# Optimization experiments

Hardware: AMD Instinct MI355X
Metric: run time of the kernel (lower is better)

## Reference

```python
import jax, jax.numpy as jnp
import numpy as np

B, C, H, W = 8, 128, 256, 256
KERNELS = [1, 3, 5]


def _dwconv(x, w, k):
    # depthwise conv, groups == channels, padding k//2 (SAME for odd k)
    return jax.lax.conv_general_dilated(
        x, w, window_strides=(1, 1),
        padding=[(k // 2, k // 2), (k // 2, k // 2)],
        dimension_numbers=("NCHW", "OIHW", "NCHW"),
        feature_group_count=x.shape[1])


def setup_inputs() -> dict:
    key = jax.random.key(0)
    ks = jax.random.split(key, 5)
    x = jax.random.normal(ks[0], (B, C, H, W), jnp.float32)
    # depthwise weights: torch layout [out_ch, in_ch/groups, k, k] = [4C, 1, k, k]
    w1 = jax.random.normal(ks[1], (4 * C, 1, 1, 1), jnp.float32) * 0.2
    w3 = jax.random.normal(ks[2], (4 * C, 1, 3, 3), jnp.float32) * 0.1
    w5 = jax.random.normal(ks[3], (4 * C, 1, 5, 5), jnp.float32) * 0.05
    # proj 1x1 conv: [4C, 12C, 1, 1]
    w_proj = jax.random.normal(ks[4], (4 * C, 12 * C, 1, 1), jnp.float32) * 0.02
    return {"x": x, "w1": w1, "w3": w3, "w5": w5, "w_proj": w_proj}


def reference(x, w1, w3, w5, w_proj):
    # DWT: strided split -> channel concat  [B,C,H,W] -> [B,4C,H/2,W/2]
    xd = jnp.concatenate([
        x[:, :, 0::2, 0::2], x[:, :, 0::2, 1::2],
        x[:, :, 1::2, 0::2], x[:, :, 1::2, 1::2]], axis=1)
    # multi-kernel depthwise convs, concat -> [B,12C,H/2,W/2]
    feats = jnp.concatenate([
        _dwconv(xd, w1, 1), _dwconv(xd, w3, 3), _dwconv(xd, w5, 5)], axis=1)
    # 1x1 projection: [B,12C,h,w] -> [B,4C,h,w]
    y = jnp.einsum("bchw,oc->bohw", feats, w_proj[:, :, 0, 0])
    # IDWT: strided zero-scatter back to [B,C,H,W]
    c = y.shape[1] // 4
    ll, lh, hl, hh = jnp.split(y, 4, axis=1)
    out = jnp.zeros((y.shape[0], c, y.shape[2] * 2, y.shape[3] * 2), y.dtype)
    out = (out.at[:, :, 0::2, 0::2].set(ll)
              .at[:, :, 0::2, 1::2].set(lh)
              .at[:, :, 1::2, 0::2].set(hl)
              .at[:, :, 1::2, 1::2].set(hh))
    return out
```

## Files before the change

### kernel.cpp

```cpp
#include <hip/hip_runtime.h>
#include <hip/hip_bf16.h>
#include <stdint.h>

typedef __bf16 bf16_t;
typedef __bf16 bf16x8 __attribute__((ext_vector_type(8)));
typedef float f32x4 __attribute__((ext_vector_type(4)));

constexpr int CC = 128, HH = 256, WW = 256;
constexpr int C4 = 512, K12 = 1536;
constexpr int AWP_ELEMS = 786432;
constexpr int LW2_ELEMS = 512 * 40;

__global__ __launch_bounds__(256)
void prep(const float* __restrict__ wp, const float* __restrict__ w1,
          const float* __restrict__ w3, const float* __restrict__ w5,
          bf16_t* __restrict__ awp, float* __restrict__ lw2g)
{
    int t = blockIdx.x * 256 + threadIdx.x;
    if (t < AWP_ELEMS) {
        int kk = t & 31, o = (t >> 5) & 511, t2 = t >> 14;
        int g = t2 >> 4, cb = t2 & 15;
        awp[t] = (bf16_t)wp[o * K12 + g * C4 + cb * 32 + kk];
        return;
    }
    int u = t - AWP_ELEMS;
    if (u < LW2_ELEMS) {
        int c4 = u / 40, j = u - c4 * 40;
        int r = j >> 3, v = j & 7;
        float val = 0.f;
        if (v < 5)                 val = w5[c4 * 25 + r * 5 + v];
        else if (r >= 1 && r <= 3) val = w3[c4 * 9 + (r - 1) * 3 + (v - 5)];
        else if (r == 0 && v == 5) val = w1[c4];
        lw2g[u] = val;
    }
}

__device__ __forceinline__ void gload4(const float* g, float* l) {
    __builtin_amdgcn_global_load_lds(
        (const __attribute__((address_space(1))) uint32_t*)g,
        (__attribute__((address_space(3))) uint32_t*)l, 4, 0, 0);
}

__device__ __forceinline__ int bt_off(int row, int colbyte) {
    int f = ((row >> 1) ^ (row >> 2)) & 7;
    return row * 256 + (colbyte ^ (f << 4));
}

__device__ __forceinline__ uint16_t b16bits(float v) {
    return __builtin_bit_cast(uint16_t, (bf16_t)v);
}

__global__ __launch_bounds__(1024, 4)
void wtconv_mfma(const float* __restrict__ x,
                 const bf16_t* __restrict__ awp,
                 const float* __restrict__ lw2g,
                 float* __restrict__ out)
{
    __shared__ __align__(16) float lx[32][5][136];
    __shared__ __align__(16) char  BtB[128 * 256];
    __shared__ __align__(16) float lw2s[2][1280];

    const int tid = threadIdx.x;
    const int lane = tid & 63;
    const int wid = __builtin_amdgcn_readfirstlane(tid >> 6);
    const int nb = blockIdx.x;
    const int m = (nb & 7) * 128 + (nb >> 3);
    const int b = m >> 7, i = m & 127;
    const int wm = wid & 7, wn = wid >> 3;
    const int lrow = lane & 15, lkh = lane >> 4;
    const float* xb = x + (size_t)b * CC * HH * WW;

    for (int e = tid; e < 32 * 5 * 136 / 4; e += 1024)
        ((f32x4*)lx)[e] = (f32x4){0.f, 0.f, 0.f, 0.f};
    __syncthreads();

    f32x4 acc[4][4];
#pragma unroll
    for (int a = 0; a < 4; ++a)
#pragma unroll
        for (int c = 0; c < 4; ++c) acc[a][c] = (f32x4){0.f, 0.f, 0.f, 0.f};

    auto issue_lx = [&](int cb) {
        const int q4 = cb >> 2;
        const int qy = q4 >> 1, qx = q4 & 1;
        const int bcb = (cb & 3) * 32;
#pragma unroll
        for (int cl = 0; cl < 2; ++cl) {
            const int chan = wid * 2 + cl;
#pragma unroll
            for (int r = 0; r < 5; ++r) {
                const int ri = i + r - 2;
                if ((unsigned)ri < 128u) {
#pragma unroll
                    for (int h = 0; h < 2; ++h) {
                        const float* s = xb + (((size_t)(bcb + chan)) << 16)
                                       + (2 * ri + qy) * WW + qx + h * 128;
                        gload4(s + 2 * lane, &lx[chan][r][2 + h * 64]);
                    }
                }
            }
        }
    };
    auto issue_lw = [&](int cb, int buf) {
        const float* src = lw2g + cb * 1280;
        float* dst = lw2s[buf];
#pragma unroll 1
        for (int t = wid; t < 20; t += 16)
            gload4(src + t * 64 + lane, dst + t * 64);
    };

    issue_lw(0, 0);
    issue_lx(0);

    const int pxq = tid & 31;
    const int chan = (tid >> 5) & 31;
    const int px0 = pxq * 4;

#pragma unroll 1
    for (int cb = 0; cb < 16; ++cb) {
        __syncthreads();

        const int buf = cb & 1;
        const float* wrow = &lw2s[buf][chan * 40];
        float f5[4] = {0.f,0.f,0.f,0.f}, f3[4] = {0.f,0.f,0.f,0.f}, f1[4];
        float w1v = 0.f;
#pragma unroll
        for (int r = 0; r < 5; ++r) {
            f32x4 wA = *(const f32x4*)(wrow + r * 8);
            f32x4 wB = *(const f32x4*)(wrow + r * 8 + 4);
            f32x4 a  = *(const f32x4*)&lx[chan][r][px0];
            f32x4 bv = *(const f32x4*)&lx[chan][r][px0 + 4];
            float col[8] = {a[0],a[1],a[2],a[3],bv[0],bv[1],bv[2],bv[3]};
            if (r == 0) w1v = wB[1];
#pragma unroll
            for (int d = 0; d < 4; ++d)
                f5[d] += wA[0]*col[d] + wA[1]*col[d+1] + wA[2]*col[d+2]
                       + wA[3]*col[d+3] + wB[0]*col[d+4];
            if (r >= 1 && r <= 3) {
#pragma unroll
                for (int d = 0; d < 4; ++d)
                    f3[d] += wB[1]*col[d+1] + wB[2]*col[d+2] + wB[3]*col[d+3];
            }
            if (r == 2) {
#pragma unroll
                for (int d = 0; d < 4; ++d) f1[d] = w1v * col[d + 2];
            }
        }
#pragma unroll
        for (int d = 0; d < 4; ++d) {
            const int row = px0 + d;
            const int cby = chan * 2;
            *(uint16_t*)&BtB[bt_off(row, cby)]       = b16bits(f1[d]);
            *(uint16_t*)&BtB[bt_off(row, 64 + cby)]  = b16bits(f3[d]);
            *(uint16_t*)&BtB[bt_off(row, 128 + cby)] = b16bits(f5[d]);
        }
        __syncthreads();

        if (cb < 15) { issue_lw(cb + 1, (cb + 1) & 1); issue_lx(cb + 1); }

#pragma unroll 1
        for (int g = 0; g < 3; ++g) {
            bf16x8 bfrag[4];
#pragma unroll
            for (int nf = 0; nf < 4; ++nf) {
                const int row = wn * 64 + nf * 16 + lrow;
                bfrag[nf] = *(const bf16x8*)&BtB[bt_off(row, g * 64 + lkh * 16)];
            }
            const bf16_t* abase = awp + (size_t)(g * 16 + cb) * (512 * 32);
#pragma unroll
            for (int mf = 0; mf < 4; ++mf) {
                const int o = wm * 64 + mf * 16 + lrow;
                bf16x8 af = *(const bf16x8*)(abase + o * 32 + lkh * 8);
#pragma unroll
                for (int nf = 0; nf < 4; ++nf)
                    acc[mf][nf] = __builtin_amdgcn_mfma_f32_16x16x32_bf16(
                        af, bfrag[nf], acc[mf][nf], 0, 0, 0);
            }
        }
    }

    const int oy = 2 * i + (wm >> 2);
    const int ox = (wm >> 1) & 1;
#pragma unroll
    for (int mf = 0; mf < 4; ++mf)
#pragma unroll
        for (int nf = 0; nf < 4; ++nf)
#pragma unroll
            for (int r = 0; r < 4; ++r) {
                const int bco = (wm & 1) * 64 + mf * 16 + lkh * 4 + r;
                const int px  = wn * 64 + nf * 16 + lrow;
                out[((size_t)(b * CC + bco) * HH + oy) * WW + 2 * px + ox]
                    = acc[mf][nf][r];
            }
}

extern "C" void kernel_launch(void* const* d_in, const int* in_sizes, int n_in,
                              void* d_out, int out_size, void* d_ws, size_t ws_size,
                              hipStream_t stream) {
    const float* x  = (const float*)d_in[0];
    const float* w1 = (const float*)d_in[1];
    const float* w3 = (const float*)d_in[2];
    const float* w5 = (const float*)d_in[3];
    const float* wp = (const float*)d_in[4];
    float* out = (float*)d_out;
    bf16_t* awp = (bf16_t*)d_ws;
    float* lw2g = (float*)((char*)d_ws + (size_t)AWP_ELEMS * 2);

    int prep_total = AWP_ELEMS + LW2_ELEMS;
    hipLaunchKernelGGL(prep, dim3((prep_total + 255) / 256), dim3(256), 0, stream,
                       wp, w1, w3, w5, awp, lw2g);
    hipLaunchKernelGGL(wtconv_mfma, dim3(1024), dim3(1024), 0, stream,
                       x, awp, lw2g, out);
}
```

Measured before the change: 536.8 us.

## Warp-specialize depthwise producer and double-buffer Bt tile to overlap with MFMA

Splits the block's waves so only the first 8 waves compute the depthwise convolutions, 8 output pixels per thread, and load the next stage's inputs. All waves run MFMA on the previous stage's tile from a double-buffered Bt LDS area, with one barrier per iteration instead of two. The projection weight layout is interleaved so the three kernel sizes of a channel sit next to each other in K, and the bf16 writes to LDS are packed into 32-bit stores. The aim is to overlap the depthwise VALU work with matrix ops and cut synchronization. In exchange it uses more LDS, which may lower occupancy, and half the waves sit idle during the depthwise phase.

```diff
diff --git a/kernel.cpp b/kernel.cpp
--- a/kernel.cpp
+++ b/kernel.cpp
@@ -9,7 +9,7 @@
 constexpr int CC = 128, HH = 256, WW = 256;
 constexpr int C4 = 512, K12 = 1536;
 constexpr int AWP_ELEMS = 786432;
-constexpr int LW2_ELEMS = 512 * 40;
+constexpr int LW2_ELEMS = 512 * 48;
 
 __global__ __launch_bounds__(256)
 void prep(const float* __restrict__ wp, const float* __restrict__ w1,
@@ -18,19 +18,23 @@
 {
     int t = blockIdx.x * 256 + threadIdx.x;
     if (t < AWP_ELEMS) {
-        int kk = t & 31, o = (t >> 5) & 511, t2 = t >> 14;
-        int g = t2 >> 4, cb = t2 & 15;
-        awp[t] = (bf16_t)wp[o * K12 + g * C4 + cb * 32 + kk];
+        int kl = t % 96;
+        int o  = (t / 96) & 511;
+        int cb = t / (96 * 512);
+        int chan = kl / 3, g = kl - chan * 3;
+        awp[t] = (bf16_t)wp[o * K12 + g * C4 + cb * 32 + chan];
         return;
     }
     int u = t - AWP_ELEMS;
     if (u < LW2_ELEMS) {
-        int c4 = u / 40, j = u - c4 * 40;
+        int c4 = u / 48, j = u - c4 * 48;
         int r = j >> 3, v = j & 7;
         float val = 0.f;
-        if (v < 5)                 val = w5[c4 * 25 + r * 5 + v];
-        else if (r >= 1 && r <= 3) val = w3[c4 * 9 + (r - 1) * 3 + (v - 5)];
-        else if (r == 0 && v == 5) val = w1[c4];
+        if (j < 40) {
+            if (v < 5)                 val = w5[c4 * 25 + r * 5 + v];
+            else if (r >= 1 && r <= 3) val = w3[c4 * 9 + (r - 1) * 3 + (v - 5)];
+            else if (r == 0 && v == 5) val = w1[c4];
+        }
         lw2g[u] = val;
     }
 }
@@ -40,14 +44,11 @@
         (const __attribute__((address_space(1))) uint32_t*)g,
         (__attribute__((address_space(3))) uint32_t*)l, 4, 0, 0);
 }
-
-__device__ __forceinline__ int bt_off(int row, int colbyte) {
-    int f = ((row >> 1) ^ (row >> 2)) & 7;
-    return row * 256 + (colbyte ^ (f << 4));
-}
-
 __device__ __forceinline__ uint16_t b16bits(float v) {
     return __builtin_bit_cast(uint16_t, (bf16_t)v);
+}
+__device__ __forceinline__ uint32_t pk2(float a, float b) {
+    return (uint32_t)b16bits(a) | ((uint32_t)b16bits(b) << 16);
 }
 
 __global__ __launch_bounds__(1024, 4)
@@ -56,9 +57,9 @@
                  const float* __restrict__ lw2g,
                  float* __restrict__ out)
 {
-    __shared__ __align__(16) float lx[32][5][136];
-    __shared__ __align__(16) char  BtB[128 * 256];
-    __shared__ __align__(16) float lw2s[2][1280];
+    __shared__ __align__(16) float lx[32][5][140];
+    __shared__ __align__(16) char  BtB[2][128 * 256];
+    __shared__ __align__(16) float lw2s[32][48];
 
     const int tid = threadIdx.x;
     const int lane = tid & 63;
@@ -70,7 +71,7 @@
     const int lrow = lane & 15, lkh = lane >> 4;
     const float* xb = x + (size_t)b * CC * HH * WW;
 
-    for (int e = tid; e < 32 * 5 * 136 / 4; e += 1024)
+    for (int e = tid; e < 32 * 5 * 140 / 4; e += 1024)
         ((f32x4*)lx)[e] = (f32x4){0.f, 0.f, 0.f, 0.f};
     __syncthreads();
 
@@ -80,101 +81,109 @@
 #pragma unroll
         for (int c = 0; c < 4; ++c) acc[a][c] = (f32x4){0.f, 0.f, 0.f, 0.f};
 
-    auto issue_lx = [&](int cb) {
-        const int q4 = cb >> 2;
-        const int qy = q4 >> 1, qx = q4 & 1;
-        const int bcb = (cb & 3) * 32;
-#pragma unroll
-        for (int cl = 0; cl < 2; ++cl) {
-            const int chan = wid * 2 + cl;
+    auto issue_own = [&](int kk) {
+        const int q4 = kk >> 2, qy = q4 >> 1, qx = q4 & 1;
+        const int bcb = (kk & 3) * 32;
+#pragma unroll
+        for (int cl = 0; cl < 4; ++cl) {
+            const int chan = wid * 4 + cl;
 #pragma unroll
             for (int r = 0; r < 5; ++r) {
                 const int ri = i + r - 2;
                 if ((unsigned)ri < 128u) {
-#pragma unroll
-                    for (int h = 0; h < 2; ++h) {
-                        const float* s = xb + (((size_t)(bcb + chan)) << 16)
-                                       + (2 * ri + qy) * WW + qx + h * 128;
-                        gload4(s + 2 * lane, &lx[chan][r][2 + h * 64]);
-                    }
-                }
-            }
-        }
+                    const float* s = xb + (((size_t)(bcb + chan)) << 16)
+                                   + (2 * ri + qy) * WW + qx;
+                    gload4(s + 2 * lane,       &lx[chan][r][2]);
+                    gload4(s + 128 + 2 * lane, &lx[chan][r][66]);
+                }
+            }
+        }
+        const float* wsrc = lw2g + kk * 1536 + wid * 192;
+        float* wdst = &lw2s[wid * 4][0];
+#pragma unroll
+        for (int t = 0; t < 3; ++t)
+            gload4(wsrc + t * 64 + lane, wdst + t * 64);
     };
-    auto issue_lw = [&](int cb, int buf) {
-        const float* src = lw2g + cb * 1280;
-        float* dst = lw2s[buf];
+
+    if (wid < 8) issue_own(0);
+
+    const int chan = (tid >> 4) & 31;
+    const int oct = tid & 15;
+    const int px0 = oct * 8;
+
 #pragma unroll 1
-        for (int t = wid; t < 20; t += 16)
-            gload4(src + t * 64 + lane, dst + t * 64);
-    };
-
-    issue_lw(0, 0);
-    issue_lx(0);
-
-    const int pxq = tid & 31;
-    const int chan = (tid >> 5) & 31;
-    const int px0 = pxq * 4;
-
-#pragma unroll 1
-    for (int cb = 0; cb < 16; ++cb) {
+    for (int k = 0; k <= 16; ++k) {
         __syncthreads();
 
-        const int buf = cb & 1;
-        const float* wrow = &lw2s[buf][chan * 40];
-        float f5[4] = {0.f,0.f,0.f,0.f}, f3[4] = {0.f,0.f,0.f,0.f}, f1[4];
-        float w1v = 0.f;
-#pragma unroll
-        for (int r = 0; r < 5; ++r) {
-            f32x4 wA = *(const f32x4*)(wrow + r * 8);
-            f32x4 wB = *(const f32x4*)(wrow + r * 8 + 4);
-            f32x4 a  = *(const f32x4*)&lx[chan][r][px0];
-            f32x4 bv = *(const f32x4*)&lx[chan][r][px0 + 4];
-            float col[8] = {a[0],a[1],a[2],a[3],bv[0],bv[1],bv[2],bv[3]};
-            if (r == 0) w1v = wB[1];
-#pragma unroll
-            for (int d = 0; d < 4; ++d)
-                f5[d] += wA[0]*col[d] + wA[1]*col[d+1] + wA[2]*col[d+2]
-                       + wA[3]*col[d+3] + wB[0]*col[d+4];
-            if (r >= 1 && r <= 3) {
-#pragma unroll
-                for (int d = 0; d < 4; ++d)
-                    f3[d] += wB[1]*col[d+1] + wB[2]*col[d+2] + wB[3]*col[d+3];
-            }
-            if (r == 2) {
-#pragma unroll
-                for (int d = 0; d < 4; ++d) f1[d] = w1v * col[d + 2];
-            }
-        }
-#pragma unroll
-        for (int d = 0; d < 4; ++d) {
-            const int row = px0 + d;
-            const int cby = chan * 2;
-            *(uint16_t*)&BtB[bt_off(row, cby)]       = b16bits(f1[d]);
-            *(uint16_t*)&BtB[bt_off(row, 64 + cby)]  = b16bits(f3[d]);
-            *(uint16_t*)&BtB[bt_off(row, 128 + cby)] = b16bits(f5[d]);
-        }
-        __syncthreads();
-
-        if (cb < 15) { issue_lw(cb + 1, (cb + 1) & 1); issue_lx(cb + 1); }
-
-#pragma unroll 1
-        for (int g = 0; g < 3; ++g) {
-            bf16x8 bfrag[4];
-#pragma unroll
-            for (int nf = 0; nf < 4; ++nf) {
-                const int row = wn * 64 + nf * 16 + lrow;
-                bfrag[nf] = *(const bf16x8*)&BtB[bt_off(row, g * 64 + lkh * 16)];
-            }
-            const bf16_t* abase = awp + (size_t)(g * 16 + cb) * (512 * 32);
-#pragma unroll
-            for (int mf = 0; mf < 4; ++mf) {
-                const int o = wm * 64 + mf * 16 + lrow;
-                bf16x8 af = *(const bf16x8*)(abase + o * 32 + lkh * 8);
-#pragma unroll
-                for (int nf = 0; nf < 4; ++nf)
-                    acc[mf][nf] = __builtin_amdgcn_mfma_f32_16x16x32_bf16(
-                        af, bfrag[nf], acc[mf][nf], 0, 0, 0);
+        if (wid < 8 && k < 16) {
+            const float* wr = &lw2s[chan][0];
+            float f5[8] = {0,0,0,0,0,0,0,0}, f3[8] = {0,0,0,0,0,0,0,0}, f1[8];
+            float w1v = 0.f;
+#pragma unroll
+            for (int r = 0; r < 5; ++r) {
+                f32x4 wA = *(const f32x4*)(wr + r * 8);
+                f32x4 wB = *(const f32x4*)(wr + r * 8 + 4);
+                f32x4 v0 = *(const f32x4*)&lx[chan][r][px0];
+                f32x4 v1 = *(const f32x4*)&lx[chan][r][px0 + 4];
+                f32x4 v2 = *(const f32x4*)&lx[chan][r][px0 + 8];
+                float c[12] = {v0[0],v0[1],v0[2],v0[3], v1[0],v1[1],v1[2],v1[3],
+                               v2[0],v2[1],v2[2],v2[3]};
+                if (r == 0) w1v = wB[1];
+#pragma unroll
+                for (int d = 0; d < 8; ++d)
+                    f5[d] += wA[0]*c[d] + wA[1]*c[d+1] + wA[2]*c[d+2]
+                           + wA[3]*c[d+3] + wB[0]*c[d+4];
+                if (r >= 1 && r <= 3) {
+#pragma unroll
+                    for (int d = 0; d < 8; ++d)
+                        f3[d] += wB[1]*c[d+1] + wB[2]*c[d+2] + wB[3]*c[d+3];
+                }
+                if (r == 2) {
+#pragma unroll
+                    for (int d = 0; d < 8; ++d) f1[d] = w1v * c[d + 2];
+                }
+            }
+            char* btb = BtB[k & 1];
+            const int odd = chan & 1;
+            const int b32off = 6 * chan + 2 * odd;
+            const int b16off = 6 * chan + 4 - 4 * odd;
+#pragma unroll
+            for (int d = 0; d < 8; ++d) {
+                const int row = px0 + d;
+                const int sw = (((row >> 1) ^ (row >> 2)) & 7) << 4;
+                char* base = btb + row * 256;
+                float lo = odd ? f3[d] : f1[d];
+                float hi = odd ? f5[d] : f3[d];
+                float sv = odd ? f1[d] : f5[d];
+                *(uint32_t*)(base + (b32off ^ sw)) = pk2(lo, hi);
+                *(uint16_t*)(base + (b16off ^ sw)) = b16bits(sv);
+            }
+            if (k < 15) issue_own(k + 1);
+        }
+
+        if (k > 0) {
+            const int prev = k - 1;
+            const char* btb = BtB[prev & 1];
+            const bf16_t* abase = awp + (size_t)prev * (512 * 96);
+#pragma unroll
+            for (int s = 0; s < 3; ++s) {
+                bf16x8 bfrag[4];
+#pragma unroll
+                for (int nf = 0; nf < 4; ++nf) {
+                    const int row = wn * 64 + nf * 16 + lrow;
+                    const int sw = (((row >> 1) ^ (row >> 2)) & 7) << 4;
+                    bfrag[nf] = *(const bf16x8*)(btb + row * 256
+                                                 + ((s * 64 + lkh * 16) ^ sw));
+                }
+#pragma unroll
+                for (int mf = 0; mf < 4; ++mf) {
+                    const int o = wm * 64 + mf * 16 + lrow;
+                    bf16x8 af = *(const bf16x8*)(abase + o * 96 + s * 32 + lkh * 8);
+#pragma unroll
+                    for (int nf = 0; nf < 4; ++nf)
+                        acc[mf][nf] = __builtin_amdgcn_mfma_f32_16x16x32_bf16(
+                            af, bfrag[nf], acc[mf][nf], 0, 0, 0);
+                }
             }
         }
     }
```

Measured after the change: 1.006 ms. +87.4%, slower.

## Double-buffer the B tile and skew depthwise conv one stage ahead of MFMA

Applied to the files above, without the earlier changes.

The B staging buffer becomes double-buffered, and the loop is restructured so that iteration k computes the depthwise conv for chunk k while the MFMA consumes chunk k-1's tile. This drops one of the two block barriers per iteration. Each wave now prefetches only its own channels' x rows and filter taps, so the next chunk's loads can be issued right after its own conv, with no barrier first. The cost is a larger LDS footprint (close to the per-CU limit) and a fully unrolled MFMA group loop, which may raise register pressure.

```diff
diff --git a/kernel.cpp b/kernel.cpp
--- a/kernel.cpp
+++ b/kernel.cpp
@@ -40,14 +40,13 @@
         (const __attribute__((address_space(1))) uint32_t*)g,
         (__attribute__((address_space(3))) uint32_t*)l, 4, 0, 0);
 }
+__device__ __forceinline__ uint16_t b16bits(float v) {
+    return __builtin_bit_cast(uint16_t, (bf16_t)v);
+}
 
 __device__ __forceinline__ int bt_off(int row, int colbyte) {
     int f = ((row >> 1) ^ (row >> 2)) & 7;
     return row * 256 + (colbyte ^ (f << 4));
-}
-
-__device__ __forceinline__ uint16_t b16bits(float v) {
-    return __builtin_bit_cast(uint16_t, (bf16_t)v);
 }
 
 __global__ __launch_bounds__(1024, 4)
@@ -57,8 +56,8 @@
                  float* __restrict__ out)
 {
     __shared__ __align__(16) float lx[32][5][136];
-    __shared__ __align__(16) char  BtB[128 * 256];
-    __shared__ __align__(16) float lw2s[2][1280];
+    __shared__ __align__(16) char  BtB[2][128 * 256];
+    __shared__ __align__(16) float lw2s[32][40];
 
     const int tid = threadIdx.x;
     const int lane = tid & 63;
@@ -80,10 +79,9 @@
 #pragma unroll
         for (int c = 0; c < 4; ++c) acc[a][c] = (f32x4){0.f, 0.f, 0.f, 0.f};
 
-    auto issue_lx = [&](int cb) {
-        const int q4 = cb >> 2;
-        const int qy = q4 >> 1, qx = q4 & 1;
-        const int bcb = (cb & 3) * 32;
+    auto issue_own = [&](int kk) {
+        const int q4 = kk >> 2, qy = q4 >> 1, qx = q4 & 1;
+        const int bcb = (kk & 3) * 32;
 #pragma unroll
         for (int cl = 0; cl < 2; ++cl) {
             const int chan = wid * 2 + cl;
@@ -91,90 +89,92 @@
             for (int r = 0; r < 5; ++r) {
                 const int ri = i + r - 2;
                 if ((unsigned)ri < 128u) {
-#pragma unroll
-                    for (int h = 0; h < 2; ++h) {
-                        const float* s = xb + (((size_t)(bcb + chan)) << 16)
-                                       + (2 * ri + qy) * WW + qx + h * 128;
-                        gload4(s + 2 * lane, &lx[chan][r][2 + h * 64]);
-                    }
+                    const float* s = xb + (((size_t)(bcb + chan)) << 16)
+                                   + (2 * ri + qy) * WW + qx;
+                    gload4(s + 2 * lane,       &lx[chan][r][2]);
+                    gload4(s + 128 + 2 * lane, &lx[chan][r][66]);
                 }
             }
         }
+        const float* wsrc = lw2g + kk * 1280 + wid * 80;
+        float* wdst = &lw2s[wid * 2][0];
+        gload4(wsrc + lane, wdst);
+        if (lane < 16) gload4(wsrc + 64 + lane, wdst + 64);
     };
-    auto issue_lw = [&](int cb, int buf) {
-        const float* src = lw2g + cb * 1280;
-        float* dst = lw2s[buf];
+
+    issue_own(0);
+
+    const int chan = tid >> 5;
+    const int pxq = tid & 31;
+    const int px0 = pxq * 4;
+
 #pragma unroll 1
-        for (int t = wid; t < 20; t += 16)
-            gload4(src + t * 64 + lane, dst + t * 64);
-    };
-
-    issue_lw(0, 0);
-    issue_lx(0);
-
-    const int pxq = tid & 31;
-    const int chan = (tid >> 5) & 31;
-    const int px0 = pxq * 4;
-
-#pragma unroll 1
-    for (int cb = 0; cb < 16; ++cb) {
+    for (int k = 0; k <= 16; ++k) {
         __syncthreads();
 
-        const int buf = cb & 1;
-        const float* wrow = &lw2s[buf][chan * 40];
-        float f5[4] = {0.f,0.f,0.f,0.f}, f3[4] = {0.f,0.f,0.f,0.f}, f1[4];
-        float w1v = 0.f;
-#pragma unroll
-        for (int r = 0; r < 5; ++r) {
-            f32x4 wA = *(const f32x4*)(wrow + r * 8);
-            f32x4 wB = *(const f32x4*)(wrow + r * 8 + 4);
-            f32x4 a  = *(const f32x4*)&lx[chan][r][px0];
-            f32x4 bv = *(const f32x4*)&lx[chan][r][px0 + 4];
-            float col[8] = {a[0],a[1],a[2],a[3],bv[0],bv[1],bv[2],bv[3]};
-            if (r == 0) w1v = wB[1];
-#pragma unroll
-            for (int d = 0; d < 4; ++d)
-                f5[d] += wA[0]*col[d] + wA[1]*col[d+1] + wA[2]*col[d+2]
-                       + wA[3]*col[d+3] + wB[0]*col[d+4];
-            if (r >= 1 && r <= 3) {
+        if (k < 16) {
+            const float* wr = &lw2s[chan][0];
+            float f5[4] = {0.f,0.f,0.f,0.f}, f3[4] = {0.f,0.f,0.f,0.f}, f1[4];
+            float w1v = 0.f;
+#pragma unroll
+            for (int r = 0; r < 5; ++r) {
+                f32x4 wA = *(const f32x4*)(wr + r * 8);
+                f32x4 wB = *(const f32x4*)(wr + r * 8 + 4);
+                f32x4 a  = *(const f32x4*)&lx[chan][r][px0];
+                f32x4 bv = *(const f32x4*)&lx[chan][r][px0 + 4];
+                float c[8] = {a[0],a[1],a[2],a[3],bv[0],bv[1],bv[2],bv[3]};
+                if (r == 0) w1v = wB[1];
 #pragma unroll
                 for (int d = 0; d < 4; ++d)
-                    f3[d] += wB[1]*col[d+1] + wB[2]*col[d+2] + wB[3]*col[d+3];
-            }
-            if (r == 2) {
-#pragma unroll
-                for (int d = 0; d < 4; ++d) f1[d] = w1v * col[d + 2];
-            }
+                    f5[d] += wA[0]*c[d] + wA[1]*c[d+1] + wA[2]*c[d+2]
+                           + wA[3]*c[d+3] + wB[0]*c[d+4];
+                if (r >= 1 && r <= 3) {
+#pragma unroll
+                    for (int d = 0; d < 4; ++d)
+                        f3[d] += wB[1]*c[d+1] + wB[2]*c[d+2] + wB[3]*c[d+3];
+                }
+                if (r == 2) {
+#pragma unroll
+                    for (int d = 0; d < 4; ++d) f1[d] = w1v * c[d + 2];
+                }
+            }
+            char* btb = BtB[k & 1];
+            const int cby = chan * 2;
+#pragma unroll
+            for (int d = 0; d < 4; ++d) {
+                const int row = px0 + d;
+                const int sw = (((row >> 1) ^ (row >> 2)) & 7) << 4;
+                char* base = btb + row * 256;
+                *(uint16_t*)(base + ((cby) ^ sw))        = b16bits(f1[d]);
+                *(uint16_t*)(base + ((64 + cby) ^ sw))   = b16bits(f3[d]);
+                *(uint16_t*)(base + ((128 + cby) ^ sw))  = b16bits(f5[d]);
+            }
+            if (k < 15) issue_own(k + 1);
         }
-#pragma unroll
-        for (int d = 0; d < 4; ++d) {
-            const int row = px0 + d;
-            const int cby = chan * 2;
-            *(uint16_t*)&BtB[bt_off(row, cby)]       = b16bits(f1[d]);
-            *(uint16_t*)&BtB[bt_off(row, 64 + cby)]  = b16bits(f3[d]);
-            *(uint16_t*)&BtB[bt_off(row, 128 + cby)] = b16bits(f5[d]);
-        }
-        __syncthreads();
-
-        if (cb < 15) { issue_lw(cb + 1, (cb + 1) & 1); issue_lx(cb + 1); }
-
-#pragma unroll 1
-        for (int g = 0; g < 3; ++g) {
-            bf16x8 bfrag[4];
-#pragma unroll
-            for (int nf = 0; nf < 4; ++nf) {
-                const int row = wn * 64 + nf * 16 + lrow;
-                bfrag[nf] = *(const bf16x8*)&BtB[bt_off(row, g * 64 + lkh * 16)];
-            }
-            const bf16_t* abase = awp + (size_t)(g * 16 + cb) * (512 * 32);
-#pragma unroll
-            for (int mf = 0; mf < 4; ++mf) {
-                const int o = wm * 64 + mf * 16 + lrow;
-                bf16x8 af = *(const bf16x8*)(abase + o * 32 + lkh * 8);
-#pragma unroll
-                for (int nf = 0; nf < 4; ++nf)
-                    acc[mf][nf] = __builtin_amdgcn_mfma_f32_16x16x32_bf16(
-                        af, bfrag[nf], acc[mf][nf], 0, 0, 0);
+
+        if (k > 0) {
+            const int prev = k - 1;
+            const char* btb = BtB[prev & 1];
+#pragma unroll
+            for (int s = 0; s < 3; ++s) {
+                bf16x8 bfrag[4];
+#pragma unroll
+                for (int nf = 0; nf < 4; ++nf) {
+                    const int row = wn * 64 + nf * 16 + lrow;
+                    const int sw = (((row >> 1) ^ (row >> 2)) & 7) << 4;
+                    bfrag[nf] = *(const bf16x8*)(btb + row * 256
+                                                 + ((s * 64 + lkh * 16) ^ sw));
+                }
+                const bf16_t* abase = awp + (size_t)(s * 16 + prev) * (512 * 32);
+#pragma unroll
+                for (int mf = 0; mf < 4; ++mf) {
+                    const int o = wm * 64 + mf * 16 + lrow;
+                    bf16x8 af = *(const bf16x8*)(abase + o * 32 + lkh * 8);
+#pragma unroll
+                    for (int nf = 0; nf < 4; ++nf)
+                        acc[mf][nf] = __builtin_amdgcn_mfma_f32_16x16x32_bf16(
+                            af, bfrag[nf], acc[mf][nf], 0, 0, 0);
+                }
             }
         }
     }
```

After: 514.8 us. 4.1% less time.
